# Kernel tuning notes

Measured on AMD Instinct MI355X. Metric: run time of the kernel, lower is better.

Reference implementation:

```python
import jax, jax.numpy as jnp
import numpy as np

H = 4      # n_heads
HD = 32    # head_dim
D = 128    # pair channels = H*HD
S = 384    # sequence length
EPS = 1e-5


def setup_inputs() -> dict:
    key = jax.random.key(0)
    ks = jax.random.split(key, 8)
    return {
        "x": jax.random.normal(ks[0], (1, S, S, D), dtype=jnp.float32),
        "attn_mask": jnp.zeros((1, 1, 1, S), dtype=jnp.float32),
        "ln_w": jax.random.uniform(ks[1], (D,), dtype=jnp.float32),
        "ln_b": jax.random.normal(ks[2], (D,), dtype=jnp.float32) * 0.02,
        "bias_w": jax.random.normal(ks[3], (H, D), dtype=jnp.float32) * 0.02,
        "qkv_w": jax.random.normal(ks[4], (3 * H * HD, D), dtype=jnp.float32) * 0.02,
        "g_w": jax.random.normal(ks[5], (H * HD, D), dtype=jnp.float32) * 0.02,
        "o_w": jax.random.normal(ks[6], (D, H * HD), dtype=jnp.float32) * 0.02,
    }


def reference(x, attn_mask, ln_w, ln_b, bias_w, qkv_w, g_w, o_w):
    # x: [1, S, S, D]; ending=False -> no permute
    xs = x[0]  # [S, S, D]; first S = batch of rows, second S = attended axis
    mu = jnp.mean(xs, axis=-1, keepdims=True)
    var = jnp.mean(jnp.square(xs - mu), axis=-1, keepdims=True)
    ln = (xs - mu) * jax.lax.rsqrt(var + EPS) * ln_w + ln_b  # [S, S, D]

    # triangle bias: D -> H, shaped [1, H, S, S], broadcast over row-batch
    bias = jnp.einsum('ijd,hd->hij', ln, bias_w)  # [H, S, S]

    # fused qkv projection, split heads
    qkv = jnp.einsum('bsd,ed->bse', ln, qkv_w)  # [S, S, 3*H*HD]
    q, k, v = jnp.split(qkv, 3, axis=-1)
    def heads(t):
        return t.reshape(S, S, H, HD).transpose(0, 2, 1, 3)  # [S, H, S, HD]
    q, k, v = heads(q), heads(k), heads(v)

    scale = 1.0 / jnp.sqrt(jnp.float32(HD))
    scores = jnp.einsum('bhqd,bhkd->bhqk', q, k) * scale  # [S, H, S, S]
    scores = scores + bias[None] + attn_mask  # attn_mask broadcasts [1,1,1,S]
    attn = jax.nn.softmax(scores, axis=-1)
    o = jnp.einsum('bhqk,bhkd->bhqd', attn, v)  # [S, H, S, HD]
    o = o.transpose(0, 2, 1, 3).reshape(S, S, H * HD)  # concat heads

    g = jnp.einsum('bsd,ed->bse', ln, g_w)  # [S, S, H*HD]
    o = o * jax.nn.sigmoid(g)
    out = jnp.einsum('bse,de->bsd', o, o_w)  # [S, S, D]
    return out[None]  # [1, S, S, D]
```

## Files before the change

### kernel.cpp

```cpp
#include <hip/hip_runtime.h>
#include <hip/hip_bf16.h>


#define S_ 384
#define D_ 128
#define MTOT (S_*S_)

typedef __bf16 bf16;
typedef __bf16 bf16x8 __attribute__((ext_vector_type(8)));
typedef __bf16 bf16x4 __attribute__((ext_vector_type(4)));
typedef float  f32x4  __attribute__((ext_vector_type(4)));

#define LOG2E      1.4426950408889634f
#define QSCALE     0.17677669529663687f
#define QSCALE_L2E 0.25505008455121566f

#if defined(__has_builtin)
#  if __has_builtin(__builtin_amdgcn_exp2f)
#    define HAVE_EXP2 1
#  else
#    define HAVE_EXP2 0
#  endif
#else
#  define HAVE_EXP2 0
#endif

#if HAVE_EXP2
#  define BIAS_MUL LOG2E
#  define Q_MUL    QSCALE_L2E
__device__ __forceinline__ float fast_pexp(float x) { return __builtin_amdgcn_exp2f(x); }
#else
#  define BIAS_MUL 1.0f
#  define Q_MUL    QSCALE
__device__ __forceinline__ float fast_pexp(float x) { return __expf(x); }
#endif

#define OFF_LN   0u
#define OFF_Q    37748736u
#define OFF_K    75497472u
#define OFF_V    113246208u
#define OFF_G    150994944u
#define OFF_BIAS 188743680u
#define OFF_W2   191102976u
#define OFF_OWB  191234048u

__global__ __launch_bounds__(256) void k0_convert(const float* __restrict__ qkv_w,
                                                  const float* __restrict__ g_w,
                                                  const float* __restrict__ o_w,
                                                  bf16* __restrict__ W2,
                                                  bf16* __restrict__ o_wb) {
    int idx = blockIdx.x * 256 + threadIdx.x;
    if (idx < 512 * 128) {
        float v = (idx < 384 * 128) ? qkv_w[idx] : g_w[idx - 384 * 128];
        W2[idx] = (bf16)v;
    }
    int idx2 = idx - 512 * 128;
    if (idx2 >= 0 && idx2 < 128 * 128) o_wb[idx2] = (bf16)o_w[idx2];
}

__global__ __launch_bounds__(256) void k1_ln(const float* __restrict__ x,
                                             const float* __restrict__ ln_w,
                                             const float* __restrict__ ln_b,
                                             const float* __restrict__ bias_w,
                                             const float* __restrict__ mask,
                                             bf16* __restrict__ ln_ws,
                                             float* __restrict__ bias_f) {
    int wid = threadIdx.x >> 6, lane = threadIdx.x & 63;
    int grp = lane >> 5, sub = lane & 31;
    int pos = blockIdx.x * 8 + wid * 2 + grp;
    f32x4 v = ((const f32x4*)(x + (size_t)pos * D_))[sub];
    float sum = v[0] + v[1] + v[2] + v[3];
    float ssq = v[0]*v[0] + v[1]*v[1] + v[2]*v[2] + v[3]*v[3];
    #pragma unroll
    for (int off = 16; off; off >>= 1) {
        sum += __shfl_xor(sum, off);
        ssq += __shfl_xor(ssq, off);
    }
    float mu   = sum * (1.0f / D_);
    float var  = ssq * (1.0f / D_) - mu * mu;
    float rstd = rsqrtf(var + 1e-5f);
    f32x4 w4 = ((const f32x4*)ln_w)[sub];
    f32x4 b4 = ((const f32x4*)ln_b)[sub];
    f32x4 y;
    #pragma unroll
    for (int i = 0; i < 4; ++i) y[i] = (v[i] - mu) * rstd * w4[i] + b4[i];
    bf16x4 yb;
    #pragma unroll
    for (int i = 0; i < 4; ++i) yb[i] = (bf16)y[i];
    *(bf16x4*)(ln_ws + (size_t)pos * D_ + 4 * sub) = yb;

    int ii = pos / S_, jj = pos - ii * S_;
    float mk = mask[jj];
    float p[4];
    #pragma unroll
    for (int h = 0; h < 4; ++h) {
        f32x4 bw = ((const f32x4*)(bias_w + h * D_))[sub];
        p[h] = y[0]*bw[0] + y[1]*bw[1] + y[2]*bw[2] + y[3]*bw[3];
    }
    #pragma unroll
    for (int off = 16; off; off >>= 1)
        #pragma unroll
        for (int h = 0; h < 4; ++h) p[h] += __shfl_xor(p[h], off);
    if (sub == 0) {
        int base = ((ii >> 4) * 24 + (jj >> 4)) * 256 + (((jj >> 2) & 3) * 16 + (ii & 15)) * 4 + (jj & 3);
        #pragma unroll
        for (int h = 0; h < 4; ++h)
            bias_f[h * 147456 + base] = (p[h] + mk) * BIAS_MUL;
    }
}

__global__ __launch_bounds__(512, 2) void k2_proj(const bf16* __restrict__ ln_ws,
                                                  const bf16* __restrict__ W2,
                                                  bf16* __restrict__ q_ws,
                                                  bf16* __restrict__ k_ws,
                                                  bf16* __restrict__ v_ws,
                                                  bf16* __restrict__ g_ws) {
    __shared__ __align__(16) char smem[128 * 272 + 128 * 272];
    char* As = smem;
    char* Bs = smem + 128 * 272;
    char* Cs = smem;
    int t = threadIdx.x;
    int bid = blockIdx.x;
    int xcd = bid & 7;
    int rem = bid >> 3;
    int by  = rem & 3;
    int bx  = ((rem >> 2) << 3) + xcd;
    int m0 = bx * 128;
    int n0 = by * 128;
    #pragma unroll
    for (int it = 0; it < 4; ++it) {
        int byte = it * 8192 + t * 16;
        int row = byte >> 8, colb = byte & 255;
        *(int4*)(As + row * 272 + colb) = *(const int4*)((const char*)ln_ws + (size_t)(m0 + row) * 256 + colb);
    }
    #pragma unroll
    for (int it = 0; it < 4; ++it) {
        int byte = it * 8192 + t * 16;
        int row = byte >> 8, colb = byte & 255;
        *(int4*)(Bs + row * 272 + colb) = *(const int4*)((const char*)W2 + (size_t)(n0 + row) * 256 + colb);
    }
    __syncthreads();
    int wid = t >> 6, lane = t & 63, lr = lane & 15, g = lane >> 4;
    int wm = wid >> 1, wn = wid & 1;
    f32x4 acc[2][4] = {};
    #pragma unroll
    for (int ks = 0; ks < 4; ++ks) {
        bf16x8 af[2], bfr[4];
        #pragma unroll
        for (int mt = 0; mt < 2; ++mt)
            af[mt] = *(const bf16x8*)(As + (wm * 32 + mt * 16 + lr) * 272 + ks * 64 + g * 16);
        #pragma unroll
        for (int nt = 0; nt < 4; ++nt)
            bfr[nt] = *(const bf16x8*)(Bs + (wn * 64 + nt * 16 + lr) * 272 + ks * 64 + g * 16);
        #pragma unroll
        for (int mt = 0; mt < 2; ++mt)
            #pragma unroll
            for (int nt = 0; nt < 4; ++nt)
                acc[mt][nt] = __builtin_amdgcn_mfma_f32_16x16x32_bf16(af[mt], bfr[nt], acc[mt][nt], 0, 0, 0);
    }
    __syncthreads();
    float cmul = (by == 0) ? Q_MUL : 1.0f;
    #pragma unroll
    for (int mt = 0; mt < 2; ++mt)
        #pragma unroll
        for (int nt = 0; nt < 4; ++nt)
            #pragma unroll
            for (int i = 0; i < 4; ++i) {
                int ml = wm * 32 + mt * 16 + g * 4 + i;
                int nl = wn * 64 + nt * 16 + lr;
                *(bf16*)(Cs + ml * 272 + nl * 2) = (bf16)(acc[mt][nt][i] * cmul);
            }
    __syncthreads();
    int b = m0 / 384;
    int jj0 = m0 - b * 384;
    if (by < 2) {
        bf16* dst0 = (by == 0) ? q_ws : k_ws;
        int h = wid >> 1, thalf = wid & 1;
        size_t bh = (size_t)b * 4 + h;
        bf16* dst = dst0 + bh * 12288 + (size_t)((jj0 >> 4) + thalf * 4) * 512 + lane * 8;
        #pragma unroll
        for (int tl = 0; tl < 4; ++tl) {
            bf16x8 v8 = *(const bf16x8*)(Cs + (thalf * 64 + tl * 16 + lr) * 272 + (h * 32 + 8 * g) * 2);
            *(bf16x8*)(dst + tl * 512) = v8;
        }
    } else if (by == 2) {
        int h = wid >> 1, vhalf = wid & 1;
        size_t bh = (size_t)b * 4 + h;
        bf16* dst = v_ws + bh * 12288 + (size_t)(jj0 >> 5) * 1024 + lane * 8;
        #pragma unroll
        for (int f = 0; f < 4; ++f) {
            int kt64 = vhalf * 2 + (f >> 1), dt = f & 1;
            bf16x8 v8;
            #pragma unroll
            for (int j = 0; j < 8; ++j) {
                int kl = 16 * (j >> 2) + 4 * g + (j & 3);
                v8[j] = *(const bf16*)(Cs + (kt64 * 32 + kl) * 272 + (h * 32 + dt * 16 + lr) * 2);
            }
            *(bf16x8*)(dst + kt64 * 1024 + dt * 512) = v8;
        }
    } else {
        #pragma unroll
        for (int j = 0; j < 4; ++j) {
            int byte = j * 8192 + t * 16;
            int ml = byte >> 8, col = byte & 255;
            *(int4*)((char*)g_ws + (size_t)(m0 + ml) * 256 + col) = *(const int4*)(Cs + ml * 272 + col);
        }
    }
}

__global__ __launch_bounds__(512, 2) void k3_attn(const bf16* __restrict__ q_ws,
                                                  const bf16* __restrict__ k_ws,
                                                  const bf16* __restrict__ v_ws,
                                                  const float* __restrict__ bias_f,
                                                  bf16* __restrict__ o_ws) {
    __shared__ __align__(16) char smem[49152];
    char* Ksh = smem;
    char* Vsh = smem + 24576;
    int t = threadIdx.x;
    int bh = blockIdx.x;
    int b = bh >> 2, h = bh & 3;
    const char* kbase = (const char*)(k_ws + (size_t)bh * 12288);
    const char* vbase = (const char*)(v_ws + (size_t)bh * 12288);
    #pragma unroll
    for (int it = 0; it < 3; ++it) {
        int byte = it * 8192 + t * 16;
        *(int4*)(Ksh + byte) = *(const int4*)(kbase + byte);
        *(int4*)(Vsh + byte) = *(const int4*)(vbase + byte);
    }
    __syncthreads();
    int wid = t >> 6, lane = t & 63, lr = lane & 15, g = lane >> 4;
    const char* qbase = (const char*)(q_ws + (size_t)bh * 12288);
    const float* bbase = bias_f + (size_t)h * 147456;
    bf16x8 qf[3];
    const f32x4* bp[3];
    #pragma unroll
    for (int u = 0; u < 3; ++u) {
        int qtile = wid + u * 8;
        qf[u] = *(const bf16x8*)(qbase + qtile * 1024 + lane * 16);
        bp[u] = (const f32x4*)(bbase + qtile * 6144) + lane;
    }
    f32x4 oa[3][2] = {};
    float lsum[3] = {0.f, 0.f, 0.f};
    #pragma unroll 1
    for (int kt = 0; kt < 4; ++kt) {
        #pragma unroll
        for (int tt = 0; tt < 3; ++tt) {
            int k0t = kt * 6 + tt * 2;
            bf16x8 kf0 = *(const bf16x8*)(Ksh + k0t * 1024 + lane * 16);
            bf16x8 kf1 = *(const bf16x8*)(Ksh + (k0t + 1) * 1024 + lane * 16);
            bf16x8 pf[3];
            #pragma unroll
            for (int u = 0; u < 3; ++u) {
                f32x4 a0 = __builtin_amdgcn_mfma_f32_16x16x32_bf16(kf0, qf[u], bp[u][k0t * 64], 0, 0, 0);
                f32x4 a1 = __builtin_amdgcn_mfma_f32_16x16x32_bf16(kf1, qf[u], bp[u][(k0t + 1) * 64], 0, 0, 0);
                #pragma unroll
                for (int i = 0; i < 4; ++i) {
                    float p0 = fast_pexp(a0[i]);
                    float p1 = fast_pexp(a1[i]);
                    lsum[u] += p0 + p1;
                    pf[u][i]     = (bf16)p0;
                    pf[u][4 + i] = (bf16)p1;
                }
            }
            const char* vb = Vsh + (kt * 3 + tt) * 2048 + lane * 16;
            bf16x8 vf0 = *(const bf16x8*)(vb);
            bf16x8 vf1 = *(const bf16x8*)(vb + 1024);
            #pragma unroll
            for (int u = 0; u < 3; ++u) {
                oa[u][0] = __builtin_amdgcn_mfma_f32_16x16x32_bf16(pf[u], vf0, oa[u][0], 0, 0, 0);
                oa[u][1] = __builtin_amdgcn_mfma_f32_16x16x32_bf16(pf[u], vf1, oa[u][1], 0, 0, 0);
            }
        }
    }
    #pragma unroll
    for (int u = 0; u < 3; ++u) {
        float l = lsum[u];
        l += __shfl_xor(l, 16);
        l += __shfl_xor(l, 32);
        float inv = 1.0f / l;
        float invq[4];
        #pragma unroll
        for (int i = 0; i < 4; ++i) invq[i] = __shfl(inv, 4 * g + i);
        int q0 = (wid + u * 8) * 16;
        #pragma unroll
        for (int dt = 0; dt < 2; ++dt)
            #pragma unroll
            for (int i = 0; i < 4; ++i)
                o_ws[((size_t)b * 384 + q0 + 4 * g + i) * 128 + h * 32 + dt * 16 + lr] = (bf16)(oa[u][dt][i] * invq[i]);
    }
}

__global__ __launch_bounds__(512, 2) void k4_out(const bf16* __restrict__ o_ws,
                                                 const bf16* __restrict__ g_ws,
                                                 const bf16* __restrict__ o_wb,
                                                 float* __restrict__ out) {
    __shared__ __align__(16) char smem[128 * 272 + 128 * 272];
    char* As = smem;
    char* Bs = smem + 128 * 272;
    int t = threadIdx.x;
    int m0 = blockIdx.x * 128;
    #pragma unroll
    for (int it = 0; it < 4; ++it) {
        int byte = it * 8192 + t * 16;
        int row = byte >> 8, colb = byte & 255;
        bf16x8 o8 = *(const bf16x8*)((const char*)o_ws + (size_t)(m0 + row) * 256 + colb);
        bf16x8 g8 = *(const bf16x8*)((const char*)g_ws + (size_t)(m0 + row) * 256 + colb);
        bf16x8 a8;
        #pragma unroll
        for (int j = 0; j < 8; ++j) {
            float ov = (float)o8[j], gv = (float)g8[j];
            a8[j] = (bf16)(ov / (1.0f + __expf(-gv)));
        }
        *(bf16x8*)(As + row * 272 + colb) = a8;
    }
    #pragma unroll
    for (int it = 0; it < 4; ++it) {
        int byte = it * 8192 + t * 16;
        int row = byte >> 8, colb = byte & 255;
        *(int4*)(Bs + row * 272 + colb) = *(const int4*)((const char*)o_wb + (size_t)row * 256 + colb);
    }
    __syncthreads();
    int wid = t >> 6, lane = t & 63, lr = lane & 15, g = lane >> 4;
    int wm = wid >> 1, wn = wid & 1;
    f32x4 acc[2][4] = {};
    #pragma unroll
    for (int ks = 0; ks < 4; ++ks) {
        bf16x8 af[2], bfr[4];
        #pragma unroll
        for (int mt = 0; mt < 2; ++mt)
            af[mt] = *(const bf16x8*)(As + (wm * 32 + mt * 16 + lr) * 272 + ks * 64 + g * 16);
        #pragma unroll
        for (int nt = 0; nt < 4; ++nt)
            bfr[nt] = *(const bf16x8*)(Bs + (wn * 64 + nt * 16 + lr) * 272 + ks * 64 + g * 16);
        #pragma unroll
        for (int mt = 0; mt < 2; ++mt)
            #pragma unroll
            for (int nt = 0; nt < 4; ++nt)
                acc[mt][nt] = __builtin_amdgcn_mfma_f32_16x16x32_bf16(af[mt], bfr[nt], acc[mt][nt], 0, 0, 0);
    }
    #pragma unroll
    for (int mt = 0; mt < 2; ++mt)
        #pragma unroll
        for (int nt = 0; nt < 4; ++nt)
            #pragma unroll
            for (int i = 0; i < 4; ++i) {
                int m = m0 + wm * 32 + mt * 16 + g * 4 + i;
                int n = wn * 64 + nt * 16 + lr;
                out[(size_t)m * 128 + n] = acc[mt][nt][i];
            }
}

extern "C" void kernel_launch(void* const* d_in, const int* in_sizes, int n_in,
                              void* d_out, int out_size, void* d_ws, size_t ws_size,
                              hipStream_t stream) {
    const float* x      = (const float*)d_in[0];
    const float* mask   = (const float*)d_in[1];
    const float* ln_w   = (const float*)d_in[2];
    const float* ln_b   = (const float*)d_in[3];
    const float* bias_w = (const float*)d_in[4];
    const float* qkv_w  = (const float*)d_in[5];
    const float* g_w    = (const float*)d_in[6];
    const float* o_w    = (const float*)d_in[7];
    char* ws = (char*)d_ws;
    bf16*  ln_ws  = (bf16*)(ws + OFF_LN);
    bf16*  q_ws   = (bf16*)(ws + OFF_Q);
    bf16*  k_ws   = (bf16*)(ws + OFF_K);
    bf16*  v_ws   = (bf16*)(ws + OFF_V);
    bf16*  g_ws   = (bf16*)(ws + OFF_G);
    float* bias_f = (float*)(ws + OFF_BIAS);
    bf16*  W2     = (bf16*)(ws + OFF_W2);
    bf16*  o_wb   = (bf16*)(ws + OFF_OWB);
    bf16*  o_ws   = ln_ws;
    float* out    = (float*)d_out;

    k0_convert<<<dim3(320), dim3(256), 0, stream>>>(qkv_w, g_w, o_w, W2, o_wb);
    k1_ln<<<dim3(MTOT / 8), dim3(256), 0, stream>>>(x, ln_w, ln_b, bias_w, mask, ln_ws, bias_f);
    k2_proj<<<dim3(MTOT / 128 * 4), dim3(512), 0, stream>>>(ln_ws, W2, q_ws, k_ws, v_ws, g_ws);
    k3_attn<<<dim3(S_ * 4), dim3(512), 0, stream>>>(q_ws, k_ws, v_ws, bias_f, o_ws);
    k4_out<<<dim3(MTOT / 128), dim3(512), 0, stream>>>(o_ws, g_ws, o_wb, out);
}
```

Baseline: 168.1 us.

## Halve attention block size, give each wave six query tiles, interleave PV MFMAs

The attention kernel now runs with 256 threads (4 waves) per block instead of 512, and each wave handles 6 query tiles instead of 3. Each K/V fragment loaded from LDS is therefore reused across twice as many query tiles. The P·V MFMAs now follow each tile's softmax directly instead of running in a separate loop. The trade-off is more registers per wave (doubled accumulators and Q fragments) and longer per-wave serial work, with occupancy relying on 4 blocks per CU.

```diff
diff --git a/kernel.cpp b/kernel.cpp
--- a/kernel.cpp
+++ b/kernel.cpp
@@ -208,7 +208,7 @@
     }
 }
 
-__global__ __launch_bounds__(512, 2) void k3_attn(const bf16* __restrict__ q_ws,
+__global__ __launch_bounds__(256, 4) void k3_attn(const bf16* __restrict__ q_ws,
                                                   const bf16* __restrict__ k_ws,
                                                   const bf16* __restrict__ v_ws,
                                                   const float* __restrict__ bias_f,
@@ -222,25 +222,21 @@
     const char* kbase = (const char*)(k_ws + (size_t)bh * 12288);
     const char* vbase = (const char*)(v_ws + (size_t)bh * 12288);
     #pragma unroll
-    for (int it = 0; it < 3; ++it) {
-        int byte = it * 8192 + t * 16;
+    for (int it = 0; it < 6; ++it) {
+        int byte = it * 4096 + t * 16;
         *(int4*)(Ksh + byte) = *(const int4*)(kbase + byte);
         *(int4*)(Vsh + byte) = *(const int4*)(vbase + byte);
     }
     __syncthreads();
     int wid = t >> 6, lane = t & 63, lr = lane & 15, g = lane >> 4;
-    const char* qbase = (const char*)(q_ws + (size_t)bh * 12288);
-    const float* bbase = bias_f + (size_t)h * 147456;
-    bf16x8 qf[3];
-    const f32x4* bp[3];
-    #pragma unroll
-    for (int u = 0; u < 3; ++u) {
-        int qtile = wid + u * 8;
-        qf[u] = *(const bf16x8*)(qbase + qtile * 1024 + lane * 16);
-        bp[u] = (const f32x4*)(bbase + qtile * 6144) + lane;
-    }
-    f32x4 oa[3][2] = {};
-    float lsum[3] = {0.f, 0.f, 0.f};
+    const char* qbase = (const char*)(q_ws + (size_t)bh * 12288) + wid * 1024 + lane * 16;
+    const f32x4* bp0 = (const f32x4*)(bias_f + (size_t)h * 147456 + wid * 6144) + lane;
+    bf16x8 qf[6];
+    #pragma unroll
+    for (int u = 0; u < 6; ++u)
+        qf[u] = *(const bf16x8*)(qbase + u * 4096);
+    f32x4 oa[6][2] = {};
+    float lsum[6] = {0.f, 0.f, 0.f, 0.f, 0.f, 0.f};
     #pragma unroll 1
     for (int kt = 0; kt < 4; ++kt) {
         #pragma unroll
@@ -248,32 +244,29 @@
             int k0t = kt * 6 + tt * 2;
             bf16x8 kf0 = *(const bf16x8*)(Ksh + k0t * 1024 + lane * 16);
             bf16x8 kf1 = *(const bf16x8*)(Ksh + (k0t + 1) * 1024 + lane * 16);
-            bf16x8 pf[3];
-            #pragma unroll
-            for (int u = 0; u < 3; ++u) {
-                f32x4 a0 = __builtin_amdgcn_mfma_f32_16x16x32_bf16(kf0, qf[u], bp[u][k0t * 64], 0, 0, 0);
-                f32x4 a1 = __builtin_amdgcn_mfma_f32_16x16x32_bf16(kf1, qf[u], bp[u][(k0t + 1) * 64], 0, 0, 0);
+            const char* vb = Vsh + (kt * 3 + tt) * 2048 + lane * 16;
+            bf16x8 vf0 = *(const bf16x8*)(vb);
+            bf16x8 vf1 = *(const bf16x8*)(vb + 1024);
+            #pragma unroll
+            for (int u = 0; u < 6; ++u) {
+                f32x4 a0 = __builtin_amdgcn_mfma_f32_16x16x32_bf16(kf0, qf[u], bp0[u * 6144 + k0t * 64], 0, 0, 0);
+                f32x4 a1 = __builtin_amdgcn_mfma_f32_16x16x32_bf16(kf1, qf[u], bp0[u * 6144 + (k0t + 1) * 64], 0, 0, 0);
+                bf16x8 pf;
                 #pragma unroll
                 for (int i = 0; i < 4; ++i) {
                     float p0 = fast_pexp(a0[i]);
                     float p1 = fast_pexp(a1[i]);
                     lsum[u] += p0 + p1;
-                    pf[u][i]     = (bf16)p0;
-                    pf[u][4 + i] = (bf16)p1;
+                    pf[i]     = (bf16)p0;
+                    pf[4 + i] = (bf16)p1;
                 }
+                oa[u][0] = __builtin_amdgcn_mfma_f32_16x16x32_bf16(pf, vf0, oa[u][0], 0, 0, 0);
+                oa[u][1] = __builtin_amdgcn_mfma_f32_16x16x32_bf16(pf, vf1, oa[u][1], 0, 0, 0);
             }
-            const char* vb = Vsh + (kt * 3 + tt) * 2048 + lane * 16;
-            bf16x8 vf0 = *(const bf16x8*)(vb);
-            bf16x8 vf1 = *(const bf16x8*)(vb + 1024);
-            #pragma unroll
-            for (int u = 0; u < 3; ++u) {
-                oa[u][0] = __builtin_amdgcn_mfma_f32_16x16x32_bf16(pf[u], vf0, oa[u][0], 0, 0, 0);
-                oa[u][1] = __builtin_amdgcn_mfma_f32_16x16x32_bf16(pf[u], vf1, oa[u][1], 0, 0, 0);
-            }
-        }
-    }
-    #pragma unroll
-    for (int u = 0; u < 3; ++u) {
+        }
+    }
+    #pragma unroll
+    for (int u = 0; u < 6; ++u) {
         float l = lsum[u];
         l += __shfl_xor(l, 16);
         l += __shfl_xor(l, 32);
@@ -281,7 +274,7 @@
         float invq[4];
         #pragma unroll
         for (int i = 0; i < 4; ++i) invq[i] = __shfl(inv, 4 * g + i);
-        int q0 = (wid + u * 8) * 16;
+        int q0 = (wid + u * 4) * 16;
         #pragma unroll
         for (int dt = 0; dt < 2; ++dt)
             #pragma unroll
@@ -376,6 +369,6 @@
     k0_convert<<<dim3(320), dim3(256), 0, stream>>>(qkv_w, g_w, o_w, W2, o_wb);
     k1_ln<<<dim3(MTOT / 8), dim3(256), 0, stream>>>(x, ln_w, ln_b, bias_w, mask, ln_ws, bias_f);
     k2_proj<<<dim3(MTOT / 128 * 4), dim3(512), 0, stream>>>(ln_ws, W2, q_ws, k_ws, v_ws, g_ws);
-    k3_attn<<<dim3(S_ * 4), dim3(512), 0, stream>>>(q_ws, k_ws, v_ws, bias_f, o_ws);
+    k3_attn<<<dim3(S_ * 4), dim3(256), 0, stream>>>(q_ws, k_ws, v_ws, bias_f, o_ws);
     k4_out<<<dim3(MTOT / 128), dim3(512), 0, stream>>>(o_ws, g_ws, o_wb, out);
 }
```

Result: slower. 236.4 us (median of 3 runs) (+40.7%).
